# Performance work log

Hardware: AMD Instinct MI355X
Metric: run time of the kernel (lower is better)

The kernel has to match this reference:

```python
import math
import jax, jax.numpy as jnp
import numpy as np

BSZ, NMAX, ENS, K = 128, 64, 4, 32
NSQ = NMAX * NMAX
N = 2 ** math.ceil(math.log2(NSQ))  # power-of-two padded size (= 4096 here)
R = BSZ * ENS
NEG = -1e30      # log-zero surrogate
LARGE = 1e10     # LARGE_NUMBER from the torch module


def log1mexp(x):
    # stable log(1 - exp(x)) for x <= 0
    x = jnp.minimum(x, -1e-7)
    big = x < -0.6931472
    xs = jnp.where(big, x, -1.0)
    xl = jnp.where(big, -1.0, x)
    return jnp.where(big, jnp.log1p(-jnp.exp(xs)), jnp.log(-jnp.expm1(xl)))


def _dp_step(carry, pi):
    # carry[r, j] = log Pr(count = j) over elements seen so far; one Bernoulli update
    lp, lq = pi  # each (R,)
    shifted = jnp.concatenate([jnp.full((carry.shape[0], 1), NEG, carry.dtype), carry[:, :-1]], axis=1)
    new = jnp.logaddexp(lp[:, None] + shifted, lq[:, None] + carry)
    return new, new


def _suffix_table(logp, logq):
    # logS[i, :, j] = log Pr(sum_{t >= i} X_t = j); shape (N+1, R, K+1)
    init = jnp.full((R, K + 1), NEG).at[:, 0].set(0.0)
    _, outs = jax.lax.scan(_dp_step, init, (logp[::-1], logq[::-1]))
    return jnp.concatenate([outs[::-1], init[None]], axis=0)


def _prefix_table(logp, logq):
    # logF[i, :, j] = log Pr(sum_{t < i} X_t = j); shape (N+1, R, K+1)
    init = jnp.full((R, K + 1), NEG).at[:, 0].set(0.0)
    _, outs = jax.lax.scan(_dp_step, init, (logp, logq))
    return jnp.concatenate([init[None], outs], axis=0)


def _sample(logp, logS, unif):
    # exact sequential sampling from the Bernoulli distribution conditioned on sum == K
    def step(r, xs):
        lp, lS_cur, lS_nxt, u = xs
        num = lp + jnp.take_along_axis(lS_nxt, jnp.clip(r - 1, 0, K)[:, None], axis=1)[:, 0]
        den = jnp.take_along_axis(lS_cur, jnp.clip(r, 0, K)[:, None], axis=1)[:, 0]
        p1 = jnp.exp(jnp.minimum(num - den, 0.0))  # Pr(X_i=1 | remaining budget r)
        x = (u < p1) & (r > 0)
        return r - x.astype(r.dtype), x
    r0 = jnp.full((R,), K, dtype=jnp.int32)
    _, xs = jax.lax.scan(step, r0, (logp, logS[:-1], logS[1:], unif))
    return xs.astype(logp.dtype).T  # (R, N) exact K-hot


def _forward(scores, unif):
    # permute/pad/logsigmoid glue exactly as the torch module
    s = scores.transpose(0, 3, 1, 2).reshape(R, NSQ)
    s = jnp.concatenate([s, jnp.full((R, N - NSQ), -LARGE, s.dtype)], axis=1)
    theta = -jax.nn.softplus(-s) + 1e-7   # logsigmoid(scores) -> log p_i
    logp = theta.T                        # (N, R)
    logq = log1mexp(theta).T              # log(1 - p_i)
    logS = _suffix_table(logp, logq)
    logF = _prefix_table(logp, logq)
    # exact k-subset marginals: mu_i = p_i * sum_j F[i,j] S[i+1, K-1-j] / Pr(total = K)
    B = jnp.flip(logS[1:], axis=-1)[..., 1:]   # (N, R, K): slot j holds logS[i+1, K-1-j]
    Bpad = jnp.concatenate([B, jnp.full(B.shape[:-1] + (1,), NEG, B.dtype)], axis=-1)
    logmu = logp + jax.nn.logsumexp(logF[:N] + Bpad, axis=-1) - logS[0, :, K]
    mu = jnp.exp(logmu).T                      # (R, N)
    hard = jax.lax.stop_gradient(_sample(logp, logS, unif.T))
    out = hard + mu - jax.lax.stop_gradient(mu)  # SIMPLE straight-through via exact marginals
    out = out[:, :NSQ].reshape(BSZ, ENS, NMAX, NMAX).transpose(0, 2, 3, 1)
    return out


def setup_inputs() -> dict:
    key = jax.random.key(0)
    k1, k2 = jax.random.split(key)
    scores = jax.random.normal(k1, (BSZ, NMAX, NMAX, ENS), dtype=jnp.float32)
    unif = jax.random.uniform(k2, (R, N), dtype=jnp.float32)
    return {"scores": scores, "unif": unif}


def reference(scores, unif):
    return _forward(scores, unif)
```

## Files before the change

kernel.cpp:

```cpp
#include <hip/hip_runtime.h>
#include <stdint.h>

#pragma clang fp contract(off)

#define NEGF (-1e30f)


__device__ __forceinline__ float xla_exp(float x) {
#pragma clang fp contract(off)
  const float exp_hi = 88.3762626647950f;
  const float exp_lo = -88.3762626647949f;
  const float LOG2EF = 1.44269504088896341f;
  const float C1 = 0.693359375f;
  const float C2 = -2.12194440e-4f;
  float xc = fminf(fmaxf(x, exp_lo), exp_hi);
  float fx = floorf(xc * LOG2EF + 0.5f);
  float tmp = fx * C1;
  float z = fx * C2;
  float xr = xc - tmp;
  xr = xr - z;
  float z2 = xr * xr;
  float y = 1.9875691500E-4f;
  y = y * xr + 1.3981999507E-3f;
  y = y * xr + 8.3334519073E-3f;
  y = y * xr + 4.1665795894E-2f;
  y = y * xr + 1.6666665459E-1f;
  y = y * xr + 5.0000001201E-1f;
  y = y * z2 + xr;
  y = y + 1.0f;
  int n = (int)fx;
  float p2n = __int_as_float((n + 127) << 23);
  float res = y * p2n;
  return fmaxf(res, x);
}

__device__ __forceinline__ float xla_exp_np(float x) {
#pragma clang fp contract(off)
  const float exp_lo = -88.3762626647949f;
  const float LOG2EF = 1.44269504088896341f;
  const float C1 = 0.693359375f;
  const float C2 = -2.12194440e-4f;
  float xc = fmaxf(x, exp_lo);
  float fx = floorf(xc * LOG2EF + 0.5f);
  float tmp = fx * C1;
  float z = fx * C2;
  float xr = xc - tmp;
  xr = xr - z;
  float z2 = xr * xr;
  float y = 1.9875691500E-4f;
  y = y * xr + 1.3981999507E-3f;
  y = y * xr + 8.3334519073E-3f;
  y = y * xr + 4.1665795894E-2f;
  y = y * xr + 1.6666665459E-1f;
  y = y * xr + 5.0000001201E-1f;
  y = y * z2 + xr;
  y = y + 1.0f;
  int n = (int)fx;
  float p2n = __int_as_float((n + 127) << 23);
  float res = y * p2n;
  return fmaxf(res, x);
}

__device__ __forceinline__ float xla_log(float xin0) {
#pragma clang fp contract(off)
  float xin = fmaxf(xin0, __int_as_float(0x00800000));
  int bits = __float_as_int(xin);
  int e_int = (bits >> 23) - 126;
  float m = __int_as_float((bits & 0x007fffff) | 0x3f000000);
  float e = (float)e_int;
  const float SQRTHF = 0.707106781186547524f;
  float mlt1 = (m < SQRTHF) ? 1.0f : 0.0f;
  float tmp2 = (m < SQRTHF) ? m : 0.0f;
  float xm = m - 1.0f;
  e = e - mlt1;
  xm = xm + tmp2;
  float z = xm * xm;
  float y = 7.0376836292E-2f;
  y = y * xm + -1.1514610310E-1f;
  y = y * xm + 1.1676998740E-1f;
  y = y * xm + -1.2420140846E-1f;
  y = y * xm + 1.4249322787E-1f;
  y = y * xm + -1.6668057665E-1f;
  y = y * xm + 2.0000714765E-1f;
  y = y * xm + -2.4999993993E-1f;
  y = y * xm + 3.3333331174E-1f;
  y = y * xm;
  y = y * z;
  y = e * -2.12194440e-4f + y;
  y = y - 0.5f * z;
  float out = xm + y;
  out = e * 0.693359375f + out;
  return out;
}

__device__ __forceinline__ float xla_log_ge1(float xin) {
#pragma clang fp contract(off)
  int bits = __float_as_int(xin);
  int e_int = (bits >> 23) - 126;
  float m = __int_as_float((bits & 0x007fffff) | 0x3f000000);
  float e = (float)e_int;
  const float SQRTHF = 0.707106781186547524f;
  float mlt1 = (m < SQRTHF) ? 1.0f : 0.0f;
  float tmp2 = (m < SQRTHF) ? m : 0.0f;
  float xm = m - 1.0f;
  e = e - mlt1;
  xm = xm + tmp2;
  float z = xm * xm;
  float y = 7.0376836292E-2f;
  y = y * xm + -1.1514610310E-1f;
  y = y * xm + 1.1676998740E-1f;
  y = y * xm + -1.2420140846E-1f;
  y = y * xm + 1.4249322787E-1f;
  y = y * xm + -1.6668057665E-1f;
  y = y * xm + 2.0000714765E-1f;
  y = y * xm + -2.4999993993E-1f;
  y = y * xm + 3.3333331174E-1f;
  y = y * xm;
  y = y * z;
  y = e * -2.12194440e-4f + y;
  y = y - 0.5f * z;
  float out = xm + y;
  out = e * 0.693359375f + out;
  return out;
}

__device__ __forceinline__ float xla_log1p(float v) {
#pragma clang fp contract(off)
  float lg = xla_log(v + 1.0f);
  float sm = (-0.5f * v + 1.0f) * v;
  return (fabsf(v) < 1e-4f) ? sm : lg;
}

__device__ __forceinline__ float xla_log1p_unit(float v) {
#pragma clang fp contract(off)
  float lg = xla_log_ge1(v + 1.0f);
  float sm = (-0.5f * v + 1.0f) * v;
  return (fabsf(v) < 1e-4f) ? sm : lg;
}

__device__ __forceinline__ float xla_expm1(float v) {
#pragma clang fp contract(off)
  float ex = xla_exp(v);
  float lgv = ex - 1.0f;
  float sm = v + (v * v) * 0.5f;
  return (fabsf(v) < 1e-5f) ? sm : lgv;
}

__device__ __forceinline__ float xla_logaddexp(float a, float b) {
#pragma clang fp contract(off)
  float amax = fmaxf(a, b);
  float delta = a - b;
  float t = xla_exp(-fabsf(delta));
  return amax + xla_log1p(t);
}

__device__ __forceinline__ float shift_up1(float x, bool fix) {
  int xi = __float_as_int(x);
  int negi = __float_as_int(NEGF);
  int a = __builtin_amdgcn_update_dpp(negi, xi, 0x111, 0xf, 0xf, false);
  int b = __builtin_amdgcn_update_dpp(negi, xi, 0x142, 0xf, 0xf, false);
  return __int_as_float(fix ? b : a);
}

__device__ __forceinline__ float rl(float v, int k) {
  return __int_as_float(__builtin_amdgcn_readlane(__float_as_int(v), k));
}

__global__ __launch_bounds__(64) void dp_kernel(
    const float* __restrict__ scores, const float* __restrict__ unif,
    float* __restrict__ out, uint32_t* __restrict__ maskws) {
#pragma clang fp contract(off)
  const int lane = threadIdx.x;
  const int r = blockIdx.x;
  const int b = r >> 2, e = r & 3;

  __shared__ uint32_t SCR[64];

  uint32_t* __restrict__ mrow = maskws + (size_t)r * 4224;

  const bool fix = (lane == 16) || (lane == 32);
  const bool elig = (lane >= 1 && lane <= 32);

  float carry = (lane == 0) ? 0.0f : NEGF;
  float pend_dd = 0.0f, pend_u = 2.0f;
  uint32_t w = 0;

#define PREP(S, TH, LQ)                                                   \
  do {                                                                    \
    float sp_ = xla_logaddexp(-(S), 0.0f);                                \
    (TH) = -sp_ + 1e-7f;                                                  \
    float xm_ = fminf((TH), -1e-7f);                                      \
    float lqa_ = xla_log1p(-xla_exp(xm_));                                \
    float lqb_ = xla_log(-xla_expm1(xm_));                                \
    (LQ) = (xm_ < -0.6931472f) ? lqa_ : lqb_;                             \
  } while (0)

  float LPc, LQc, Uc;
  {
    float s0 = scores[((size_t)b * 4096 + 4032 + lane) * 4 + e];
    Uc = unif[(size_t)r * 4096 + 4032 + lane];
    PREP(s0, LPc, LQc);
  }

  float LPn = 0.0f, LQn = 0.0f, Un_hold = 0.0f;

#pragma unroll 1
  for (int t = 0; t < 64; ++t) {
    const int bn = 4032 - 64 * t;
    float Sn = 0.0f, Un = 0.0f;
    if (t < 63) {
      Sn = scores[((size_t)b * 4096 + (bn - 64) + lane) * 4 + e];
      Un = unif[(size_t)r * 4096 + (bn - 64) + lane];
    }
#pragma unroll
    for (int k = 63; k >= 0; --k) {
      {
        float p1 = xla_exp_np(fminf(pend_dd, 0.0f));
        bool bit = elig && (pend_u < p1);
        unsigned long long bm = __ballot(bit);
        uint32_t m32 = (uint32_t)(bm >> 1);
        const int slot = (k + 1) & 63;
        w = (lane == slot) ? m32 : w;
        if (k == 63) mrow[(unsigned)((bn + 64) >> 6) * 64 + lane] = w;
      }
      if (k == 32 && t < 63) {
        PREP(Sn, LPn, LQn);
        Un_hold = Un;
      }
      {
        float lp = rl(LPc, k);
        float lq = rl(LQc, k);
        float u = rl(Uc, k);
        float sh = shift_up1(carry, fix);
        float x1 = lp + sh;
        float x2 = lq + carry;
        float amax = fmaxf(x1, x2);
        float delta = x1 - x2;
        float E = xla_exp_np(-fabsf(delta));
        float l = xla_log1p_unit(E);
        float nv = amax + l;
        pend_dd = x1 - nv;
        pend_u = u;
        carry = nv;
      }
    }
    if (t < 63) {
      LPc = LPn;
      LQc = LQn;
      Uc = Un_hold;
    }
  }
  {
    float p1 = xla_exp_np(fminf(pend_dd, 0.0f));
    bool bit = elig && (pend_u < p1);
    unsigned long long bm = __ballot(bit);
    uint32_t m32 = (uint32_t)(bm >> 1);
    w = (lane == 0) ? m32 : w;
    mrow[lane] = w;
  }

#undef PREP

  __threadfence();

  int rb = 32;
#pragma unroll 1
  for (int g = 0; g < 64; ++g) {
    uint32_t mw = __hip_atomic_load(&mrow[g * 64 + lane], __ATOMIC_RELAXED,
                                    __HIP_MEMORY_SCOPE_AGENT);
    SCR[lane] = mw;
    __builtin_amdgcn_s_barrier();
    float myv = 0.0f;
#pragma unroll
    for (int q = 0; q < 64; ++q) {
      uint32_t mm = SCR[q];
      uint32_t bit = (rb > 0) ? ((mm >> ((rb - 1) & 31)) & 1u) : 0u;
      myv = ((lane == q) && bit) ? 1.0f : myv;
      rb -= (int)bit;
    }
    __builtin_amdgcn_s_barrier();
    out[((size_t)(b * 64 + g) * 64 + lane) * 4 + e] = myv;
  }
}

extern "C" void kernel_launch(void* const* d_in, const int* in_sizes, int n_in,
                              void* d_out, int out_size, void* d_ws,
                              size_t ws_size, hipStream_t stream) {
  (void)in_sizes; (void)n_in; (void)out_size; (void)ws_size;
  const float* scores = (const float*)d_in[0];
  const float* unif = (const float*)d_in[1];
  float* out = (float*)d_out;
  uint32_t* maskws = (uint32_t*)d_ws;

  dp_kernel<<<512, 64, 0, stream>>>(scores, unif, out, maskws);
}
```

Before: 1.220 ms.

## Merge sampling exp into DP-step exp via idle upper lanes and lane rotation

Lanes 1-32 keep running the logaddexp DP, while lanes 33-63 (and lane 0) now compute the sampling probability exp in the same exp call. Each sees the previous step's pend_dd rotated across the wave halves by a shuffle, so the separate per-step exp for sampling goes away. The ballot mask is rebuilt from the upper half plus lane 0. Other changes: the inner 64-step loop becomes 8 outer by 8 unrolled steps, PREP moves to block granularity, the exp drops its final fmax, and the log's mantissa test becomes an integer compare. The risks are an extra cross-lane shuffle on the serial dependency chain and subtle lane-mapping correctness.

Result: faster. 1.089 ms (-10.8%).

```diff
diff --git a/kernel.cpp b/kernel.cpp
--- a/kernel.cpp
+++ b/kernel.cpp
@@ -34,7 +34,7 @@
   return fmaxf(res, x);
 }
 
-__device__ __forceinline__ float xla_exp_np(float x) {
+__device__ __forceinline__ float xla_exp_nt(float x) {
 #pragma clang fp contract(off)
   const float exp_lo = -88.3762626647949f;
   const float LOG2EF = 1.44269504088896341f;
@@ -57,8 +57,7 @@
   y = y + 1.0f;
   int n = (int)fx;
   float p2n = __int_as_float((n + 127) << 23);
-  float res = y * p2n;
-  return fmaxf(res, x);
+  return y * p2n;
 }
 
 __device__ __forceinline__ float xla_log(float xin0) {
@@ -93,15 +92,15 @@
   return out;
 }
 
-__device__ __forceinline__ float xla_log_ge1(float xin) {
-#pragma clang fp contract(off)
-  int bits = __float_as_int(xin);
-  int e_int = (bits >> 23) - 126;
-  float m = __int_as_float((bits & 0x007fffff) | 0x3f000000);
-  float e = (float)e_int;
-  const float SQRTHF = 0.707106781186547524f;
-  float mlt1 = (m < SQRTHF) ? 1.0f : 0.0f;
-  float tmp2 = (m < SQRTHF) ? m : 0.0f;
+__device__ __forceinline__ float xla_log_ge1u(float xin) {
+#pragma clang fp contract(off)
+  uint32_t bits = __float_as_uint(xin);
+  uint32_t f = bits & 0x007fffffu;
+  float m = __uint_as_float(f | 0x3f000000u);
+  float e = (float)(int)((bits >> 23) - 126u);
+  bool cl = f < 0x003504F3u;
+  float mlt1 = cl ? 1.0f : 0.0f;
+  float tmp2 = cl ? m : 0.0f;
   float xm = m - 1.0f;
   e = e - mlt1;
   xm = xm + tmp2;
@@ -133,7 +132,7 @@
 
 __device__ __forceinline__ float xla_log1p_unit(float v) {
 #pragma clang fp contract(off)
-  float lg = xla_log_ge1(v + 1.0f);
+  float lg = xla_log_ge1u(v + 1.0f);
   float sm = (-0.5f * v + 1.0f) * v;
   return (fabsf(v) < 1e-4f) ? sm : lg;
 }
@@ -179,10 +178,12 @@
   uint32_t* __restrict__ mrow = maskws + (size_t)r * 4224;
 
   const bool fix = (lane == 16) || (lane == 32);
-  const bool elig = (lane >= 1 && lane <= 32);
-
-  float carry = (lane == 0) ? 0.0f : NEGF;
-  float pend_dd = 0.0f, pend_u = 2.0f;
+  const bool is_chain = (lane >= 1 && lane <= 32);
+  const bool is_l0 = (lane == 0);
+
+  float carry = is_l0 ? 0.0f : NEGF;
+  float pend_dd = NEGF;
+  float pend_u = 2.0f;
   uint32_t w = 0;
 
 #define PREP(S, TH, LQ)                                                   \
@@ -203,6 +204,7 @@
   }
 
   float LPn = 0.0f, LQn = 0.0f, Un_hold = 0.0f;
+  float rot_pend = __shfl(pend_dd, lane ^ 32);
 
 #pragma unroll 1
   for (int t = 0; t < 64; ++t) {
@@ -212,22 +214,12 @@
       Sn = scores[((size_t)b * 4096 + (bn - 64) + lane) * 4 + e];
       Un = unif[(size_t)r * 4096 + (bn - 64) + lane];
     }
+#pragma unroll 1
+    for (int kb = 7; kb >= 0; --kb) {
 #pragma unroll
-    for (int k = 63; k >= 0; --k) {
-      {
-        float p1 = xla_exp_np(fminf(pend_dd, 0.0f));
-        bool bit = elig && (pend_u < p1);
-        unsigned long long bm = __ballot(bit);
-        uint32_t m32 = (uint32_t)(bm >> 1);
-        const int slot = (k + 1) & 63;
-        w = (lane == slot) ? m32 : w;
-        if (k == 63) mrow[(unsigned)((bn + 64) >> 6) * 64 + lane] = w;
-      }
-      if (k == 32 && t < 63) {
-        PREP(Sn, LPn, LQn);
-        Un_hold = Un;
-      }
-      {
+      for (int kk = 7; kk >= 0; --kk) {
+        const int k = kb * 8 + kk;
+        float finv = fminf(rot_pend, 0.0f);
         float lp = rl(LPc, k);
         float lq = rl(LQc, k);
         float u = rl(Uc, k);
@@ -236,12 +228,25 @@
         float x2 = lq + carry;
         float amax = fmaxf(x1, x2);
         float delta = x1 - x2;
-        float E = xla_exp_np(-fabsf(delta));
+        float ein = is_chain ? (-fabsf(delta)) : finv;
+        float E = xla_exp_nt(ein);
+        unsigned long long bm = __ballot(pend_u < E);
+        uint32_t m32 = (uint32_t)(bm >> 33) | (((uint32_t)bm & 1u) << 31);
+        const int slot = (k + 1) & 63;
+        w = (lane == slot) ? m32 : w;
+        if (kk == 7 && kb == 7)
+          mrow[(unsigned)((bn + 64) >> 6) * 64 + lane] = w;
         float l = xla_log1p_unit(E);
         float nv = amax + l;
+        nv = is_l0 ? x2 : nv;
         pend_dd = x1 - nv;
+        rot_pend = __shfl(pend_dd, lane ^ 32);
         pend_u = u;
         carry = nv;
+      }
+      if (kb == 4 && t < 63) {
+        PREP(Sn, LPn, LQn);
+        Un_hold = Un;
       }
     }
     if (t < 63) {
@@ -251,10 +256,9 @@
     }
   }
   {
-    float p1 = xla_exp_np(fminf(pend_dd, 0.0f));
-    bool bit = elig && (pend_u < p1);
-    unsigned long long bm = __ballot(bit);
-    uint32_t m32 = (uint32_t)(bm >> 1);
+    float E = xla_exp_nt(fminf(rot_pend, 0.0f));
+    unsigned long long bm = __ballot(pend_u < E);
+    uint32_t m32 = (uint32_t)(bm >> 33) | (((uint32_t)bm & 1u) << 31);
     w = (lane == 0) ? m32 : w;
     mrow[lane] = w;
   }
```
